# Performance work log

Hardware: AMD Instinct MI355X
Metric: run time of the kernel (lower is better)

## Reference

```python
import jax, jax.numpy as jnp
import numpy as np

R = 512  # rnn_size == att_hid_size == input_encoding_size


def _forward(seq, att_feats, embed_w, W_word, b_word, W_h, b_h, W_img, b_img,
             W_ae, b_ae, W_c2a, b_c2a, W_sl, b_sl, W_se, b_se,
             W_hl, b_hl, W_he, b_he, W_al, b_al, W_a2h, b_a2h, W_log, b_log):
    B, T = seq.shape
    # att_embed: Linear(2048->512) + ReLU  (dropout = identity in eval)
    af = jax.nn.relu(att_feats @ W_ae + b_ae)            # [B,196,R]
    p_att = af @ W_c2a + b_c2a                            # [B,196,R] precomputed attention keys
    img_gate = af.mean(axis=1) @ W_img + b_img            # [B,6R] image contribution to gates (constant over t)
    x_emb = jax.nn.relu(embed_w[seq[:, :T - 1]])          # [B,T-1,R] word embeddings
    wg_t = jnp.swapaxes(x_emb @ W_word + b_word, 0, 1)    # [T-1,B,6R]

    def step(carry, wg):
        hx, cx = carry
        gates = wg + hx @ W_h + b_h + img_gate            # [B,6R]
        sig = jax.nn.sigmoid(gates[:, :4 * R])
        i_g = sig[:, :R]
        f_g = sig[:, R:2 * R]
        o_g = sig[:, 2 * R:3 * R]
        s_g = sig[:, 3 * R:4 * R]
        cell = jnp.maximum(gates[:, 4 * R:5 * R], gates[:, 5 * R:6 * R])
        cy = jnp.tanh(f_g * cx + i_g * cell)
        sent = s_g * cy                                   # visual sentinel
        hy = o_g * cy
        # AdaAttention
        sent_lin = jax.nn.relu(sent @ W_sl + b_sl)        # [B,R]
        sent_emb = sent_lin @ W_se + b_se
        h_lin = jnp.tanh(hy @ W_hl + b_hl)
        h_emb = h_lin @ W_he + b_he
        img_all = jnp.concatenate([sent_lin[:, None, :], af], axis=1)        # [B,197,R]
        img_all_emb = jnp.concatenate([sent_emb[:, None, :], p_att], axis=1)  # [B,197,R]
        hA = jnp.tanh(img_all_emb + h_emb[:, None, :])
        alpha = jax.nn.softmax((hA @ W_al + b_al)[..., 0], axis=-1)           # [B,197]
        cHat = jnp.einsum('ba,bad->bd', alpha, img_all)
        out = jnp.tanh((cHat + h_lin) @ W_a2h + b_a2h)    # [B,R]
        logp = jax.nn.log_softmax(out @ W_log + b_log, axis=-1)  # [B,V]
        return (hy, cy), logp

    h0 = jnp.zeros((B, R), att_feats.dtype)
    _, logps = jax.lax.scan(step, (h0, h0), wg_t)
    return jnp.swapaxes(logps, 0, 1)                      # [B,T-1,V]


def setup_inputs() -> dict:
    B, T, A, FEAT, V = 64, 21, 196, 2048, 7800
    cnt = [0]
    def nk():
        cnt[0] += 1
        return jax.random.fold_in(jax.random.key(0), cnt[0])
    def p(*shape):
        return jax.random.normal(nk(), shape, jnp.float32) * 0.02
    return dict(
        seq=jax.random.randint(nk(), (B, T), 0, V),
        att_feats=jax.random.normal(nk(), (B, A, FEAT), jnp.float32),
        embed_w=p(V, R),
        W_word=p(R, 6 * R), b_word=p(6 * R),
        W_h=p(R, 6 * R), b_h=p(6 * R),
        W_img=p(R, 6 * R), b_img=p(6 * R),
        W_ae=p(FEAT, R), b_ae=p(R),
        W_c2a=p(R, R), b_c2a=p(R),
        W_sl=p(R, R), b_sl=p(R),
        W_se=p(R, R), b_se=p(R),
        W_hl=p(R, R), b_hl=p(R),
        W_he=p(R, R), b_he=p(R),
        W_al=p(R, 1), b_al=p(1),
        W_a2h=p(R, R), b_a2h=p(R),
        W_log=p(R, V), b_log=p(V),
    )


def reference(seq, att_feats, embed_w, W_word, b_word, W_h, b_h, W_img, b_img,
              W_ae, b_ae, W_c2a, b_c2a, W_sl, b_sl, W_se, b_se,
              W_hl, b_hl, W_he, b_he, W_al, b_al, W_a2h, b_a2h, W_log, b_log):
    return _forward(seq, att_feats, embed_w, W_word, b_word, W_h, b_h, W_img, b_img,
                    W_ae, b_ae, W_c2a, b_c2a, W_sl, b_sl, W_se, b_se,
                    W_hl, b_hl, W_he, b_he, W_al, b_al, W_a2h, b_a2h, W_log, b_log)
```

## Files before the change

kernel.cpp:

```cpp
#include <hip/hip_runtime.h>

using short8 = __attribute__((ext_vector_type(8))) short;
using f32x4  = __attribute__((ext_vector_type(4))) float;
typedef unsigned short u16;
typedef unsigned int u32;

__device__ __forceinline__ float b2f(u16 u){
    return __uint_as_float(((u32)u) << 16);
}
__device__ __forceinline__ u16 f2b(float f){
    u32 x = __float_as_uint(f);
    u32 r = (x + 0x7FFFu + ((x >> 16) & 1u)) >> 16;
    return (u16)r;
}
__device__ __forceinline__ float ldx(const void* p, size_t i, bool f32){
    return f32 ? ((const float*)p)[i] : b2f(((const u16*)p)[i]);
}
__device__ __forceinline__ float sigf(float x){
    return __builtin_amdgcn_rcpf(1.0f + __expf(-x));
}
__device__ __forceinline__ float tanhf_(float x){
    float e = __expf(2.0f*x);
    return 1.0f - 2.0f*__builtin_amdgcn_rcpf(e + 1.0f);
}

#define GLDS(g, l) __builtin_amdgcn_global_load_lds((const __attribute__((address_space(1))) void*)(g), \
                        (__attribute__((address_space(3))) void*)(l), 16, 0, 0)

__global__ void probe_dtype(const void* w, int* flag){
    const u16* up = (const u16*)w;
    int lane = threadIdx.x & 63;
    int cnt = 0;
    for (int i = lane; i < 256; i += 64){
        u16 u = up[2*i];
        int e = (u >> 7) & 0xFF;
        if (e >= 100 && e <= 126) cnt++;
    }
    #pragma unroll
    for (int off = 32; off; off >>= 1) cnt += __shfl_xor(cnt, off);
    if (lane == 0) *flag = (cnt >= 192) ? 0 : 1;
}

__global__ __launch_bounds__(256) void convert_att(const void* __restrict__ in, u16* __restrict__ out,
                                                   const int* __restrict__ dflag, int total8){
    bool f32 = (*dflag != 0);
    int i = blockIdx.x*256 + threadIdx.x;
    if (i >= total8) return;
    size_t e = (size_t)i*8;
    if (f32){
        const float4* p = (const float4*)((const float*)in + e);
        float4 v0 = p[0], v1 = p[1];
        u16 o[8] = { f2b(v0.x),f2b(v0.y),f2b(v0.z),f2b(v0.w),
                     f2b(v1.x),f2b(v1.y),f2b(v1.z),f2b(v1.w) };
        *(uint4*)(out + e) = *(const uint4*)o;
    } else {
        *(uint4*)(out + e) = *(const uint4*)((const u16*)in + e);
    }
}

struct TP { const void* src[8]; u16* dst[8]; };
__global__ __launch_bounds__(256) void transpose_multi(TP tp, int K, int N, int Npad,
                                                       const int* __restrict__ dflag){
    __shared__ u16 tile[32][33];
    bool f32 = (*dflag != 0);
    const void* in = tp.src[blockIdx.z];
    u16* out = tp.dst[blockIdx.z];
    int bx = blockIdx.x, by = blockIdx.y;
    int tx = threadIdx.x, ty = threadIdx.y;
    int n = bx*32 + tx;
    #pragma unroll
    for (int i = 0; i < 32; i += 8){
        int k = by*32 + ty + i;
        u16 v = 0;
        if (n < N && k < K)
            v = f32 ? f2b(((const float*)in)[(size_t)k*N + n]) : ((const u16*)in)[(size_t)k*N + n];
        tile[ty+i][tx] = v;
    }
    __syncthreads();
    int k2 = by*32 + tx;
    #pragma unroll
    for (int i = 0; i < 32; i += 8){
        int n2 = bx*32 + ty + i;
        if (n2 < Npad && k2 < K) out[(size_t)n2*K + k2] = tile[tx][ty+i];
    }
}

__global__ __launch_bounds__(256) void gather_emb(const int* __restrict__ seq, const void* __restrict__ embed,
                                                  u16* __restrict__ x_emb, const int* __restrict__ dflag){
    bool f32 = (*dflag != 0);
    int idx = blockIdx.x*256 + threadIdx.x;
    if (idx >= 1280*512) return;
    int row = idx >> 9, r = idx & 511;
    int b = row / 20, t = row % 20;
    int w = seq[b*21 + t];
    float v = ldx(embed, (size_t)w*512 + r, f32);
    x_emb[idx] = f2b(fmaxf(v, 0.f));
}

__global__ __launch_bounds__(256) void mean_af_kernel(const u16* __restrict__ af, u16* __restrict__ mean_af){
    int b = blockIdx.x, tid = threadIdx.x;
    for (int r = tid; r < 512; r += 256){
        float s = 0.f;
        for (int a = 0; a < 196; ++a) s += b2f(af[((size_t)(b*196+a))*512 + r]);
        mean_af[b*512+r] = f2b(s * (1.0f/196.0f));
    }
}

template<int TM>
__global__ __launch_bounds__(256) void gemm_tn(const u16* __restrict__ A, const u16* __restrict__ BT,
                                               int N, int K,
                                               const void* __restrict__ bias1, const void* __restrict__ bias2,
                                               const float* __restrict__ rowAdd, int rowDiv,
                                               float* __restrict__ Cf, u16* __restrict__ Cb,
                                               int act, int Nvalid, int Mvalid,
                                               const int* __restrict__ dflag, int perm){
    constexpr int MW = TM/64;
    __shared__ u16 As[TM*64];
    __shared__ u16 Bs[64*64];
    bool f32 = (*dflag != 0);
    int tid = threadIdx.x, lane = tid & 63, w = tid >> 6;
    int lr = lane & 15, kq = lane >> 4;

    int gN = gridDim.x;
    int nwg = gN * gridDim.y;
    int flat = blockIdx.y*gN + blockIdx.x;
    int q = nwg >> 3, r = nwg & 7;
    int xcd = flat & 7, pos = flat >> 3;
    int wgid = (xcd < r ? xcd*(q+1) : r*(q+1) + (xcd-r)*q) + pos;
    int bm = wgid / gN, bn = wgid % gN;
    int row0 = bm*TM, col0 = bn*64;

    f32x4 acc[MW][4];
    #pragma unroll
    for (int m=0;m<MW;++m)
        #pragma unroll
        for (int n=0;n<4;++n) acc[m][n] = (f32x4){0.f,0.f,0.f,0.f};

    for (int k0 = 0; k0 < K; k0 += 64){
        #pragma unroll
        for (int i=0;i<TM/32;++i){
            int c = i*256 + tid;
            int row = c>>3, slot = (c&7) ^ (row&7);
            GLDS((const char*)A + ((size_t)(row0+row)*K + k0)*2 + slot*16,
                 As + (size_t)(i*256 + w*64)*8);
        }
        #pragma unroll
        for (int i=0;i<2;++i){
            int c = i*256 + tid;
            int row = c>>3, slot = (c&7) ^ (row&7);
            GLDS((const char*)BT + ((size_t)(col0+row)*K + k0)*2 + slot*16,
                 Bs + (size_t)(i*256 + w*64)*8);
        }
        __syncthreads();
        short8 av[MW][2], bv[4][2];
        #pragma unroll
        for (int ks=0;ks<2;++ks){
            #pragma unroll
            for (int m=0;m<MW;++m){
                int rrow = w*(TM/4) + m*16 + lr;
                int sl = (ks*4+kq) ^ (rrow&7);
                av[m][ks] = *(const short8*)(As + rrow*64 + sl*8);
            }
            #pragma unroll
            for (int n=0;n<4;++n){
                int rrow = n*16 + lr;
                int sl = (ks*4+kq) ^ (rrow&7);
                bv[n][ks] = *(const short8*)(Bs + rrow*64 + sl*8);
            }
        }
        #pragma unroll
        for (int ks=0;ks<2;++ks)
            #pragma unroll
            for (int m=0;m<MW;++m)
                #pragma unroll
                for (int n=0;n<4;++n)
                    acc[m][n] = __builtin_amdgcn_mfma_f32_16x16x32_bf16(av[m][ks], bv[n][ks], acc[m][n], 0,0,0);
        __syncthreads();
    }

    #pragma unroll
    for (int n=0;n<4;++n){
        int col = col0 + n*16 + lr;
        float bvv = 0.f;
        if (col < Nvalid){
            if (bias1) bvv += ldx(bias1, col, f32);
            if (bias2) bvv += ldx(bias2, col, f32);
        }
        #pragma unroll
        for (int m=0;m<MW;++m){
            #pragma unroll
            for (int rr=0;rr<4;++rr){
                int row = row0 + w*(TM/4) + m*16 + kq*4 + rr;
                if (row < Mvalid && col < Nvalid){
                    float v = acc[m][n][rr] + bvv;
                    if (rowAdd) v += rowAdd[(size_t)(row/rowDiv)*N + col];
                    if (act == 1) v = fmaxf(v, 0.f);
                    else if (act == 2) v = tanhf_(v);
                    size_t o;
                    if (perm){
                        int orow = (row % 20)*64 + row/20;
                        int ocol = (col & 511)*6 + (col >> 9);
                        o = (size_t)orow*N + ocol;
                    } else {
                        o = (size_t)row*N + col;
                    }
                    if (Cf) Cf[o] = v;
                    if (Cb) Cb[o] = f2b(v);
                }
            }
        }
    }
}

struct GP { const u16* A; const u16* BT; const void* b1; float* Cf; u16* Cb; int act; };
struct GP2 { GP g[2]; };
__global__ __launch_bounds__(256) void gemm_tn2(GP2 ps, int N, int K, int Nvalid, int Mvalid,
                                                const int* __restrict__ dflag){
    __shared__ u16 As[64*64];
    __shared__ u16 Bs[64*64];
    bool f32 = (*dflag != 0);
    GP gp = ps.g[blockIdx.z];
    int tid = threadIdx.x, lane = tid & 63, w = tid >> 6;
    int lr = lane & 15, kq = lane >> 4;

    int gN = gridDim.x;
    int nwg = gN * gridDim.y;
    int flat = blockIdx.y*gN + blockIdx.x;
    int q = nwg >> 3, r = nwg & 7;
    int xcd = flat & 7, pos = flat >> 3;
    int wgid = (xcd < r ? xcd*(q+1) : r*(q+1) + (xcd-r)*q) + pos;
    int bm = wgid / gN, bn = wgid % gN;
    int row0 = bm*64, col0 = bn*64;

    f32x4 acc[4];
    #pragma unroll
    for (int n=0;n<4;++n) acc[n] = (f32x4){0.f,0.f,0.f,0.f};

    for (int k0 = 0; k0 < K; k0 += 64){
        {
            int c = tid;
            int row = c>>3, slot = (c&7) ^ (row&7);
            GLDS((const char*)gp.A + ((size_t)(row0+row)*K + k0)*2 + slot*16,
                 As + (size_t)(w*64)*8);
            c = 256 + tid;
            row = c>>3; slot = (c&7) ^ (row&7);
            GLDS((const char*)gp.A + ((size_t)(row0+row)*K + k0)*2 + slot*16,
                 As + (size_t)(256 + w*64)*8);
            c = tid;
            row = c>>3; slot = (c&7) ^ (row&7);
            GLDS((const char*)gp.BT + ((size_t)(col0+row)*K + k0)*2 + slot*16,
                 Bs + (size_t)(w*64)*8);
            c = 256 + tid;
            row = c>>3; slot = (c&7) ^ (row&7);
            GLDS((const char*)gp.BT + ((size_t)(col0+row)*K + k0)*2 + slot*16,
                 Bs + (size_t)(256 + w*64)*8);
        }
        __syncthreads();
        short8 av[2], bv[4][2];
        #pragma unroll
        for (int ks=0;ks<2;++ks){
            int rrow = w*16 + lr;
            int sl = (ks*4+kq) ^ (rrow&7);
            av[ks] = *(const short8*)(As + rrow*64 + sl*8);
            #pragma unroll
            for (int n=0;n<4;++n){
                int rr2 = n*16 + lr;
                int sl2 = (ks*4+kq) ^ (rr2&7);
                bv[n][ks] = *(const short8*)(Bs + rr2*64 + sl2*8);
            }
        }
        #pragma unroll
        for (int ks=0;ks<2;++ks)
            #pragma unroll
            for (int n=0;n<4;++n)
                acc[n] = __builtin_amdgcn_mfma_f32_16x16x32_bf16(av[ks], bv[n][ks], acc[n], 0,0,0);
        __syncthreads();
    }

    #pragma unroll
    for (int n=0;n<4;++n){
        int col = col0 + n*16 + lr;
        float bvv = (col < Nvalid && gp.b1) ? ldx(gp.b1, col, f32) : 0.f;
        #pragma unroll
        for (int rr=0;rr<4;++rr){
            int row = row0 + w*16 + kq*4 + rr;
            if (row < Mvalid && col < Nvalid){
                float v = acc[n][rr] + bvv;
                if (gp.act == 1) v = fmaxf(v, 0.f);
                else if (gp.act == 2) v = tanhf_(v);
                size_t o = (size_t)row*N + col;
                if (gp.Cf) gp.Cf[o] = v;
                if (gp.Cb) gp.Cb[o] = f2b(v);
            }
        }
    }
}

#define GP3 52
__global__ __launch_bounds__(192) void lstm_step(const u16* __restrict__ h_in, const u16* __restrict__ WT_h,
                                                 const float* __restrict__ wgb, float* __restrict__ cstate,
                                                 u16* __restrict__ h_out, u16* __restrict__ sent_all,
                                                 u16* __restrict__ hy_all, int t){
    __shared__ float gates[16*GP3];
    int tid = threadIdx.x, lane = tid & 63, w = tid >> 6;
    int mg = blockIdx.x >> 6, rg = blockIdx.x & 63;
    int b0 = mg*16, r0 = rg*8;
    int lr = lane & 15, kq = lane >> 4, kg = kq*8;
    int c = w*16 + lr;
    int gate = c >> 3, rcol = r0 + (c & 7);
    const u16* Ap = h_in + (size_t)(b0 + lr)*512 + kg;
    const u16* Bp = WT_h + ((size_t)gate*512 + rcol)*512 + kg;
    f32x4 acc = (f32x4){0.f,0.f,0.f,0.f};
    #pragma unroll
    for (int k0 = 0; k0 < 512; k0 += 32){
        short8 a  = *(const short8*)(Ap + k0);
        short8 bf = *(const short8*)(Bp + k0);
        acc = __builtin_amdgcn_mfma_f32_16x16x32_bf16(a, bf, acc, 0,0,0);
    }
    #pragma unroll
    for (int rr = 0; rr < 4; ++rr)
        gates[(kq*4+rr)*GP3 + c] = acc[rr];
    __syncthreads();
    if (tid < 128){
        int ri = tid >> 3, rr = tid & 7;
        int b = b0 + ri, r = r0 + rr;
        const float* wp = wgb + (((size_t)t*64 + b)*512 + r)*6;
        float2 w01 = *(const float2*)(wp);
        float2 w23 = *(const float2*)(wp + 2);
        float2 w45 = *(const float2*)(wp + 4);
        float g0 = gates[ri*GP3 +      rr] + w01.x;
        float g1 = gates[ri*GP3 +  8 + rr] + w01.y;
        float g2 = gates[ri*GP3 + 16 + rr] + w23.x;
        float g3 = gates[ri*GP3 + 24 + rr] + w23.y;
        float g4 = gates[ri*GP3 + 32 + rr] + w45.x;
        float g5 = gates[ri*GP3 + 40 + rr] + w45.y;
        float ig = sigf(g0), fg = sigf(g1), og = sigf(g2), sg = sigf(g3);
        float cell = fmaxf(g4, g5);
        float co = cstate[b*512 + r];
        float cy = tanhf_(fg*co + ig*cell);
        cstate[b*512 + r] = cy;
        float sent = sg*cy, hy = og*cy;
        h_out[(size_t)b*512 + r] = f2b(hy);
        size_t rgl = (size_t)b*20 + t;
        sent_all[rgl*512 + r] = f2b(sent);
        hy_all[rgl*512 + r]   = f2b(hy);
    }
}

__global__ __launch_bounds__(256) void attn_kernel(const u16* __restrict__ sembb, const float* __restrict__ h_emb,
                                                   const float* __restrict__ sent_lin_f, const float* __restrict__ h_lin_f,
                                                   const u16* __restrict__ p_att, const u16* __restrict__ af,
                                                   const void* __restrict__ W_al, const void* __restrict__ b_al,
                                                   u16* __restrict__ ctx_in, const int* __restrict__ dflag){
    __shared__ float he_s[512];
    __shared__ float wal_s[512];
    __shared__ float se_s[512];
    __shared__ float ev[208];
    __shared__ float red2[2];
    bool f32 = (*dflag != 0);
    int flat = blockIdx.x;
    int row = (flat & 7)*160 + (flat >> 3);
    int b = row / 20;
    int tid = threadIdx.x, lane = tid & 63, w = tid >> 6;
    for (int d = tid; d < 512; d += 256){
        int ad = ((d & 7) >> 1)*128 + (d >> 3)*2 + (d & 1);
        he_s[ad]  = h_emb[(size_t)row*512 + d];
        wal_s[ad] = ldx(W_al, d, f32);
        se_s[ad]  = b2f(sembb[(size_t)row*512 + d]);
    }
    __syncthreads();
    float bal = ldx(b_al, 0, f32);

    if (w == 0){
        float p0 = 0.f;
        #pragma unroll
        for (int jp = 0; jp < 4; ++jp){
            float2 he2 = *(const float2*)&he_s[jp*128 + lane*2];
            float2 wa2 = *(const float2*)&wal_s[jp*128 + lane*2];
            float2 se2 = *(const float2*)&se_s[jp*128 + lane*2];
            p0 += tanhf_(se2.x + he2.x) * wa2.x;
            p0 += tanhf_(se2.y + he2.y) * wa2.y;
        }
        #pragma unroll
        for (int off = 32; off; off >>= 1) p0 += __shfl_xor(p0, off);
        if (lane == 0) ev[0] = p0 + bal;
    }

    const u16* pb = p_att + (size_t)b*196*512 + lane*8;
    for (int a = 1 + w; a < 197; a += 8){
        bool has2 = (a + 4 < 197);
        const u16* r0 = pb + (size_t)(a-1)*512;
        short8 v0 = *(const short8*)r0;
        short8 v1 = has2 ? *(const short8*)(r0 + (size_t)4*512) : v0;
        const u32* pk0 = (const u32*)&v0;
        const u32* pk1 = (const u32*)&v1;
        float p0 = 0.f, p1 = 0.f;
        #pragma unroll
        for (int jp = 0; jp < 4; ++jp){
            float2 he2 = *(const float2*)&he_s[jp*128 + lane*2];
            float2 wa2 = *(const float2*)&wal_s[jp*128 + lane*2];
            u32 u0 = pk0[jp], u1 = pk1[jp];
            float x00 = __uint_as_float(u0 << 16)          + he2.x;
            float x01 = __uint_as_float(u0 & 0xFFFF0000u)  + he2.y;
            float x10 = __uint_as_float(u1 << 16)          + he2.x;
            float x11 = __uint_as_float(u1 & 0xFFFF0000u)  + he2.y;
            p0 += tanhf_(x00)*wa2.x;
            p0 += tanhf_(x01)*wa2.y;
            p1 += tanhf_(x10)*wa2.x;
            p1 += tanhf_(x11)*wa2.y;
        }
        #pragma unroll
        for (int off = 32; off; off >>= 1){
            p0 += __shfl_xor(p0, off);
            p1 += __shfl_xor(p1, off);
        }
        if (lane == 0){
            ev[a] = p0 + bal;
            if (has2) ev[a+4] = p1 + bal;
        }
    }
    __syncthreads();

    if (w == 0){
        float m = -1e30f;
        for (int a = lane; a < 197; a += 64) m = fmaxf(m, ev[a]);
        #pragma unroll
        for (int off = 32; off; off >>= 1) m = fmaxf(m, __shfl_xor(m, off));
        float s = 0.f;
        for (int a = lane; a < 197; a += 64) s += __expf(ev[a] - m);
        #pragma unroll
        for (int off = 32; off; off >>= 1) s += __shfl_xor(s, off);
        if (lane == 0){ red2[0] = m; red2[1] = __builtin_amdgcn_rcpf(s); }
    }
    __syncthreads();
    float m = red2[0], inv = red2[1];
    for (int a = tid; a < 197; a += 256) ev[a] = __expf(ev[a] - m) * inv;
    __syncthreads();

    int d = tid*2;
    const u16* afb = af + (size_t)b*196*512 + d;
    float s0 = 0.f, s1 = 0.f, t0 = 0.f, t1 = 0.f;
    for (int a = 0; a < 196; a += 2){
        float e0 = ev[a+1], e1 = ev[a+2];
        u32 u0 = *(const u32*)(afb + (size_t)a*512);
        u32 u1 = *(const u32*)(afb + (size_t)(a+1)*512);
        s0 += e0 * __uint_as_float(u0 << 16);
        s1 += e0 * __uint_as_float(u0 & 0xFFFF0000u);
        t0 += e1 * __uint_as_float(u1 << 16);
        t1 += e1 * __uint_as_float(u1 & 0xFFFF0000u);
    }
    float e00 = ev[0];
    float a0 = e00*sent_lin_f[(size_t)row*512 + d]     + s0 + t0 + h_lin_f[(size_t)row*512 + d];
    float a1 = e00*sent_lin_f[(size_t)row*512 + d + 1] + s1 + t1 + h_lin_f[(size_t)row*512 + d + 1];
    ctx_in[(size_t)row*512 + d]     = f2b(a0);
    ctx_in[(size_t)row*512 + d + 1] = f2b(a1);
}

__global__ __launch_bounds__(256) void logsoftmax_kernel(const u16* __restrict__ logits, void* __restrict__ out,
                                                         const int* __restrict__ dflag){
    __shared__ float red[256];
    bool f32 = (*dflag != 0);
    int row = blockIdx.x, tid = threadIdx.x;
    const u16* lp = logits + (size_t)row*7808;
    float m = -1e30f;
    for (int v = tid; v < 7800; v += 256) m = fmaxf(m, b2f(lp[v]));
    red[tid] = m; __syncthreads();
    for (int s = 128; s; s >>= 1){ if (tid < s) red[tid] = fmaxf(red[tid], red[tid+s]); __syncthreads(); }
    m = red[0]; __syncthreads();
    float s = 0.f;
    for (int v = tid; v < 7800; v += 256) s += __expf(b2f(lp[v]) - m);
    red[tid] = s; __syncthreads();
    for (int st = 128; st; st >>= 1){ if (tid < st) red[tid] += red[tid+st]; __syncthreads(); }
    float lse = m + __logf(red[0]);
    if (f32){
        float* op = (float*)out + (size_t)row*7800;
        for (int v = tid; v < 7800; v += 256) op[v] = b2f(lp[v]) - lse;
    } else {
        u16* op = (u16*)out + (size_t)row*7800;
        for (int v = tid; v < 7800; v += 256) op[v] = f2b(b2f(lp[v]) - lse);
    }
}

extern "C" void kernel_launch(void* const* d_in, const int* in_sizes, int n_in,
                              void* d_out, int out_size, void* d_ws, size_t ws_size,
                              hipStream_t stream){
    (void)in_sizes; (void)n_in; (void)out_size; (void)ws_size;
    const int* seq    = (const int*)d_in[0];
    const void* att   = d_in[1];
    const void* embed = d_in[2];
    const void* W_word= d_in[3];  const void* b_word = d_in[4];
    const void* W_h   = d_in[5];  const void* b_h    = d_in[6];
    const void* W_img = d_in[7];  const void* b_img  = d_in[8];
    const void* W_ae  = d_in[9];  const void* b_ae   = d_in[10];
    const void* W_c2a = d_in[11]; const void* b_c2a  = d_in[12];
    const void* W_sl  = d_in[13]; const void* b_sl   = d_in[14];
    const void* W_se  = d_in[15]; const void* b_se   = d_in[16];
    const void* W_hl  = d_in[17]; const void* b_hl   = d_in[18];
    const void* W_he  = d_in[19]; const void* b_he   = d_in[20];
    const void* W_al  = d_in[21]; const void* b_al   = d_in[22];
    const void* W_a2h = d_in[23]; const void* b_a2h  = d_in[24];
    const void* W_log = d_in[25]; const void* b_log  = d_in[26];

    char* p = (char*)d_ws;
    auto alloc = [&](size_t bytes)->char*{ char* r = p; p += (bytes + 255) & ~(size_t)255; return r; };

    int* dflag   = (int*)alloc(256);
    u16* WT_ae   = (u16*)alloc((size_t)512*2048*2);
    u16* WT_word = (u16*)alloc((size_t)3072*512*2);
    u16* WT_h    = (u16*)alloc((size_t)3072*512*2);
    u16* WT_img  = (u16*)alloc((size_t)3072*512*2);
    u16* WT_c2a  = (u16*)alloc((size_t)512*512*2);
    u16* WT_sl   = (u16*)alloc((size_t)512*512*2);
    u16* WT_se   = (u16*)alloc((size_t)512*512*2);
    u16* WT_hl   = (u16*)alloc((size_t)512*512*2);
    u16* WT_he   = (u16*)alloc((size_t)512*512*2);
    u16* WT_a2h  = (u16*)alloc((size_t)512*512*2);
    u16* WT_log  = (u16*)alloc((size_t)7808*512*2);
    u16* af      = (u16*)alloc((size_t)12544*512*2);
    u16* p_att   = (u16*)alloc((size_t)12544*512*2);
    u16* meanb   = (u16*)alloc((size_t)64*512*2);
    float* imgg  = (float*)alloc((size_t)64*3072*4);
    u16* xemb    = (u16*)alloc((size_t)1280*512*2);
    float* wgb   = (float*)alloc((size_t)1280*3072*4);
    u16* hb0     = (u16*)alloc((size_t)64*512*2);
    u16* hb1     = (u16*)alloc((size_t)64*512*2);
    float* cst   = (float*)alloc((size_t)64*512*4);
    u16* sent_all= (u16*)alloc((size_t)1280*512*2);
    u16* hy_all  = (u16*)alloc((size_t)1280*512*2);
    float* slf   = (float*)alloc((size_t)1280*512*4);
    u16* slb     = (u16*)alloc((size_t)1280*512*2);
    float* hlf   = (float*)alloc((size_t)1280*512*4);
    u16* hlb     = (u16*)alloc((size_t)1280*512*2);
    u16* sembb   = (u16*)alloc((size_t)1280*512*2);
    float* hemb  = (float*)alloc((size_t)1280*512*4);
    u16* ctx     = (u16*)alloc((size_t)1280*512*2);
    u16* a2hb    = (u16*)alloc((size_t)1280*512*2);
    u16* logits  = (u16*)alloc((size_t)1280*7808*2);

    u16* attb = (u16*)wgb;

    probe_dtype<<<1, 64, 0, stream>>>(W_ae, dflag);

    dim3 tb(32,8);
    {
        TP t6{};
        t6.src[0]=W_c2a; t6.dst[0]=WT_c2a;
        t6.src[1]=W_sl;  t6.dst[1]=WT_sl;
        t6.src[2]=W_se;  t6.dst[2]=WT_se;
        t6.src[3]=W_hl;  t6.dst[3]=WT_hl;
        t6.src[4]=W_he;  t6.dst[4]=WT_he;
        t6.src[5]=W_a2h; t6.dst[5]=WT_a2h;
        transpose_multi<<<dim3(16,16,6), tb, 0, stream>>>(t6, 512, 512, 512, dflag);
        TP t3{};
        t3.src[0]=W_word; t3.dst[0]=WT_word;
        t3.src[1]=W_h;    t3.dst[1]=WT_h;
        t3.src[2]=W_img;  t3.dst[2]=WT_img;
        transpose_multi<<<dim3(96,16,3), tb, 0, stream>>>(t3, 512, 3072, 3072, dflag);
        TP ta{}; ta.src[0]=W_ae; ta.dst[0]=WT_ae;
        transpose_multi<<<dim3(16,64,1), tb, 0, stream>>>(ta, 2048, 512, 512, dflag);
        TP tl{}; tl.src[0]=W_log; tl.dst[0]=WT_log;
        transpose_multi<<<dim3(244,16,1), tb, 0, stream>>>(tl, 512, 7800, 7808, dflag);
    }

    convert_att<<<12544, 256, 0, stream>>>(att, attb, dflag, 12544*2048/8);

    gemm_tn<128><<<dim3(8,98), 256, 0, stream>>>(attb, WT_ae, 512, 2048,
                                                 b_ae, nullptr, nullptr, 1, nullptr, af, 1, 512, 12544, dflag, 0);
    gemm_tn<128><<<dim3(8,98), 256, 0, stream>>>(af, WT_c2a, 512, 512,
                                                 b_c2a, nullptr, nullptr, 1, nullptr, p_att, 0, 512, 12544, dflag, 0);
    mean_af_kernel<<<64, 256, 0, stream>>>(af, meanb);
    gemm_tn<64><<<dim3(48,1), 256, 0, stream>>>(meanb, WT_img, 3072, 512,
                                                b_img, nullptr, nullptr, 1, imgg, nullptr, 0, 3072, 64, dflag, 0);
    gather_emb<<<2560, 256, 0, stream>>>(seq, embed, xemb, dflag);
    gemm_tn<64><<<dim3(48,20), 256, 0, stream>>>(xemb, WT_word, 3072, 512,
                                                 b_word, b_h, imgg, 20, wgb, nullptr, 0, 3072, 1280, dflag, 1);

    hipMemsetAsync(hb0, 0, (size_t)64*512*2, stream);
    hipMemsetAsync(cst, 0, (size_t)64*512*4, stream);

    for (int t = 0; t < 20; ++t){
        const u16* hin = (t & 1) ? hb1 : hb0;
        u16* hout      = (t & 1) ? hb0 : hb1;
        lstm_step<<<256, 192, 0, stream>>>(hin, WT_h, wgb, cst, hout, sent_all, hy_all, t);
    }

    GP2 pa{};
    pa.g[0] = { sent_all, WT_sl, b_sl, slf, slb, 1 };
    pa.g[1] = { hy_all,   WT_hl, b_hl, hlf, hlb, 2 };
    gemm_tn2<<<dim3(8,20,2), 256, 0, stream>>>(pa, 512, 512, 512, 1280, dflag);
    GP2 pb{};
    pb.g[0] = { slb, WT_se, b_se, nullptr, sembb, 0 };
    pb.g[1] = { hlb, WT_he, b_he, hemb, nullptr, 0 };
    gemm_tn2<<<dim3(8,20,2), 256, 0, stream>>>(pb, 512, 512, 512, 1280, dflag);

    attn_kernel<<<1280, 256, 0, stream>>>(sembb, hemb, slf, hlf, p_att, af, W_al, b_al, ctx, dflag);
    gemm_tn<64><<<dim3(8,20), 256, 0, stream>>>(ctx, WT_a2h, 512, 512,
                                                b_a2h, nullptr, nullptr, 1, nullptr, a2hb, 2, 512, 1280, dflag, 0);
    gemm_tn<128><<<dim3(122,10), 256, 0, stream>>>(a2hb, WT_log, 7808, 512,
                                                   b_log, nullptr, nullptr, 1, nullptr, logits, 0, 7800, 1280, dflag, 0);
    logsoftmax_kernel<<<1280, 256, 0, stream>>>(logits, d_out, dflag);
}
```

Before: 423.3 us.

## Fuse fp32-to-bf16 conversion into att_embed GEMM, tabulate tanh, cache logits

Removes the separate convert_att pass. A new gemm_af kernel loads fp32 att_feats straight into LDS and packs them to bf16 in registers before the MFMA, which saves a full write and reread of the large converted buffer. The attention kernel replaces its exp-based tanh with a 512-entry LDS lookup table and linear interpolation. The log-softmax kernel keeps each row's logits in registers so the row is read once instead of three times. The table-based tanh is an approximation that loses some accuracy, and the new GEMM uses 64-row tiles without software pipelining, which may cost GEMM efficiency.

```diff
diff --git a/kernel.cpp b/kernel.cpp
--- a/kernel.cpp
+++ b/kernel.cpp
@@ -22,6 +22,11 @@
 __device__ __forceinline__ float tanhf_(float x){
     float e = __expf(2.0f*x);
     return 1.0f - 2.0f*__builtin_amdgcn_rcpf(e + 1.0f);
+}
+__device__ __forceinline__ u32 cvtpk(float lo, float hi){
+    u32 r;
+    asm("v_cvt_pk_bf16_f32 %0, %1, %2" : "=v"(r) : "v"(lo), "v"(hi));
+    return r;
 }
 
 #define GLDS(g, l) __builtin_amdgcn_global_load_lds((const __attribute__((address_space(1))) void*)(g), \
@@ -39,23 +44,6 @@
     #pragma unroll
     for (int off = 32; off; off >>= 1) cnt += __shfl_xor(cnt, off);
     if (lane == 0) *flag = (cnt >= 192) ? 0 : 1;
-}
-
-__global__ __launch_bounds__(256) void convert_att(const void* __restrict__ in, u16* __restrict__ out,
-                                                   const int* __restrict__ dflag, int total8){
-    bool f32 = (*dflag != 0);
-    int i = blockIdx.x*256 + threadIdx.x;
-    if (i >= total8) return;
-    size_t e = (size_t)i*8;
-    if (f32){
-        const float4* p = (const float4*)((const float*)in + e);
-        float4 v0 = p[0], v1 = p[1];
-        u16 o[8] = { f2b(v0.x),f2b(v0.y),f2b(v0.z),f2b(v0.w),
-                     f2b(v1.x),f2b(v1.y),f2b(v1.z),f2b(v1.w) };
-        *(uint4*)(out + e) = *(const uint4*)o;
-    } else {
-        *(uint4*)(out + e) = *(const uint4*)((const u16*)in + e);
-    }
 }
 
 struct TP { const void* src[8]; u16* dst[8]; };
@@ -103,6 +91,112 @@
         float s = 0.f;
         for (int a = 0; a < 196; ++a) s += b2f(af[((size_t)(b*196+a))*512 + r]);
         mean_af[b*512+r] = f2b(s * (1.0f/196.0f));
+    }
+}
+
+__global__ __launch_bounds__(256) void gemm_af(const void* __restrict__ A, const u16* __restrict__ BT,
+                                               int N, int K, const void* __restrict__ bias1,
+                                               u16* __restrict__ Cb, int Nvalid, int Mvalid,
+                                               const int* __restrict__ dflag){
+    __shared__ char AsRaw[64*64*4];
+    __shared__ u16 Bs[64*64];
+    bool f32 = (*dflag != 0);
+    float* Asf = (float*)AsRaw;
+    u16* As16 = (u16*)AsRaw;
+    int tid = threadIdx.x, lane = tid & 63, w = tid >> 6;
+    int lr = lane & 15, kq = lane >> 4;
+
+    int gN = gridDim.x;
+    int nwg = gN * gridDim.y;
+    int flat = blockIdx.y*gN + blockIdx.x;
+    int q = nwg >> 3, r = nwg & 7;
+    int xcd = flat & 7, pos = flat >> 3;
+    int wgid = (xcd < r ? xcd*(q+1) : r*(q+1) + (xcd-r)*q) + pos;
+    int bm = wgid / gN, bn = wgid % gN;
+    int row0 = bm*64, col0 = bn*64;
+
+    f32x4 acc[4];
+    #pragma unroll
+    for (int n=0;n<4;++n) acc[n] = (f32x4){0.f,0.f,0.f,0.f};
+
+    for (int k0 = 0; k0 < K; k0 += 64){
+        if (f32){
+            const float* Af = (const float*)A;
+            #pragma unroll
+            for (int i=0;i<4;++i){
+                int c = i*256 + tid;
+                int row = c >> 4, sslot = c & 15;
+                int srcslot = sslot ^ ((row & 7) << 1);
+                GLDS((const char*)(Af + (size_t)(row0+row)*K + k0) + srcslot*16,
+                     Asf + (size_t)(i*256 + w*64)*4);
+            }
+        } else {
+            const u16* Ab = (const u16*)A;
+            #pragma unroll
+            for (int i=0;i<2;++i){
+                int c = i*256 + tid;
+                int row = c>>3, slot = (c&7) ^ (row&7);
+                GLDS((const char*)(Ab + (size_t)(row0+row)*K + k0) + slot*16,
+                     As16 + (size_t)(i*256 + w*64)*8);
+            }
+        }
+        #pragma unroll
+        for (int i=0;i<2;++i){
+            int c = i*256 + tid;
+            int row = c>>3, slot = (c&7) ^ (row&7);
+            GLDS((const char*)BT + ((size_t)(col0+row)*K + k0)*2 + slot*16,
+                 Bs + (size_t)(i*256 + w*64)*8);
+        }
+        __syncthreads();
+        short8 av[2], bv[4][2];
+        int rrow = w*16 + lr;
+        if (f32){
+            int m8 = (rrow & 7) << 1;
+            #pragma unroll
+            for (int ks=0;ks<2;++ks){
+                int j = ks*4 + kq;
+                float4 lo = *(const float4*)&Asf[rrow*64 + ((2*j)^m8)*4];
+                float4 hi = *(const float4*)&Asf[rrow*64 + ((2*j+1)^m8)*4];
+                u32 pk[4] = { cvtpk(lo.x,lo.y), cvtpk(lo.z,lo.w),
+                              cvtpk(hi.x,hi.y), cvtpk(hi.z,hi.w) };
+                av[ks] = *(const short8*)pk;
+            }
+        } else {
+            #pragma unroll
+            for (int ks=0;ks<2;++ks){
+                int sl = (ks*4+kq) ^ (rrow&7);
+                av[ks] = *(const short8*)(As16 + rrow*64 + sl*8);
+            }
+        }
+        #pragma unroll
+        for (int ks=0;ks<2;++ks){
+            #pragma unroll
+            for (int n=0;n<4;++n){
+                int rr2 = n*16 + lr;
+                int sl2 = (ks*4+kq) ^ (rr2&7);
+                bv[n][ks] = *(const short8*)(Bs + rr2*64 + sl2*8);
+            }
+        }
+        #pragma unroll
+        for (int ks=0;ks<2;++ks)
+            #pragma unroll
+            for (int n=0;n<4;++n)
+                acc[n] = __builtin_amdgcn_mfma_f32_16x16x32_bf16(av[ks], bv[n][ks], acc[n], 0,0,0);
+        __syncthreads();
+    }
+
+    #pragma unroll
+    for (int n=0;n<4;++n){
+        int col = col0 + n*16 + lr;
+        float bvv = (col < Nvalid && bias1) ? ldx(bias1, col, f32) : 0.f;
+        #pragma unroll
+        for (int rr=0;rr<4;++rr){
+            int row = row0 + w*16 + kq*4 + rr;
+            if (row < Mvalid && col < Nvalid){
+                float v = fmaxf(acc[n][rr] + bvv, 0.f);
+                Cb[(size_t)row*N + col] = f2b(v);
+            }
+        }
     }
 }
 
@@ -352,6 +446,7 @@
                                                    const u16* __restrict__ p_att, const u16* __restrict__ af,
                                                    const void* __restrict__ W_al, const void* __restrict__ b_al,
                                                    u16* __restrict__ ctx_in, const int* __restrict__ dflag){
+    __shared__ float tab[512];
     __shared__ float he_s[512];
     __shared__ float wal_s[512];
     __shared__ float se_s[512];
@@ -362,6 +457,8 @@
     int row = (flat & 7)*160 + (flat >> 3);
     int b = row / 20;
     int tid = threadIdx.x, lane = tid & 63, w = tid >> 6;
+    #pragma unroll
+    for (int i = tid; i < 512; i += 256) tab[i] = tanhf((i - 256) * 0.03125f);
     for (int d = tid; d < 512; d += 256){
         int ad = ((d & 7) >> 1)*128 + (d >> 3)*2 + (d & 1);
         he_s[ad]  = h_emb[(size_t)row*512 + d];
@@ -371,6 +468,15 @@
     __syncthreads();
     float bal = ldx(b_al, 0, f32);
 
+    auto tanh_t = [&](float x)->float{
+        float xc = fminf(fmaxf(x, -7.9f), 7.9f);
+        float fi = __fmaf_rn(xc, 32.0f, 256.0f);
+        int ii = (int)fi;
+        float fr = fi - (float)ii;
+        float t0 = tab[ii], t1 = tab[ii+1];
+        return __fmaf_rn(fr, t1 - t0, t0);
+    };
+
     if (w == 0){
         float p0 = 0.f;
         #pragma unroll
@@ -378,8 +484,8 @@
             float2 he2 = *(const float2*)&he_s[jp*128 + lane*2];
             float2 wa2 = *(const float2*)&wal_s[jp*128 + lane*2];
             float2 se2 = *(const float2*)&se_s[jp*128 + lane*2];
-            p0 += tanhf_(se2.x + he2.x) * wa2.x;
-            p0 += tanhf_(se2.y + he2.y) * wa2.y;
+            p0 += tanh_t(se2.x + he2.x) * wa2.x;
+            p0 += tanh_t(se2.y + he2.y) * wa2.y;
         }
         #pragma unroll
         for (int off = 32; off; off >>= 1) p0 += __shfl_xor(p0, off);
@@ -404,10 +510,10 @@
             float x01 = __uint_as_float(u0 & 0xFFFF0000u)  + he2.y;
             float x10 = __uint_as_float(u1 << 16)          + he2.x;
             float x11 = __uint_as_float(u1 & 0xFFFF0000u)  + he2.y;
-            p0 += tanhf_(x00)*wa2.x;
-            p0 += tanhf_(x01)*wa2.y;
-            p1 += tanhf_(x10)*wa2.x;
-            p1 += tanhf_(x11)*wa2.y;
+            p0 += tanh_t(x00)*wa2.x;
+            p0 += tanh_t(x01)*wa2.y;
+            p1 += tanh_t(x10)*wa2.x;
+            p1 += tanh_t(x11)*wa2.y;
         }
         #pragma unroll
         for (int off = 32; off; off >>= 1){
@@ -462,22 +568,37 @@
     bool f32 = (*dflag != 0);
     int row = blockIdx.x, tid = threadIdx.x;
     const u16* lp = logits + (size_t)row*7808;
+    float xs[31];
     float m = -1e30f;
-    for (int v = tid; v < 7800; v += 256) m = fmaxf(m, b2f(lp[v]));
+    #pragma unroll
+    for (int k = 0; k < 31; ++k){
+        int v = k*256 + tid;
+        xs[k] = (v < 7800) ? b2f(lp[v]) : -1e30f;
+        m = fmaxf(m, xs[k]);
+    }
     red[tid] = m; __syncthreads();
     for (int s = 128; s; s >>= 1){ if (tid < s) red[tid] = fmaxf(red[tid], red[tid+s]); __syncthreads(); }
     m = red[0]; __syncthreads();
     float s = 0.f;
-    for (int v = tid; v < 7800; v += 256) s += __expf(b2f(lp[v]) - m);
+    #pragma unroll
+    for (int k = 0; k < 31; ++k) s += __expf(xs[k] - m);
     red[tid] = s; __syncthreads();
     for (int st = 128; st; st >>= 1){ if (tid < st) red[tid] += red[tid+st]; __syncthreads(); }
     float lse = m + __logf(red[0]);
     if (f32){
         float* op = (float*)out + (size_t)row*7800;
-        for (int v = tid; v < 7800; v += 256) op[v] = b2f(lp[v]) - lse;
+        #pragma unroll
+        for (int k = 0; k < 31; ++k){
+            int v = k*256 + tid;
+            if (v < 7800) op[v] = xs[k] - lse;
+        }
     } else {
         u16* op = (u16*)out + (size_t)row*7800;
-        for (int v = tid; v < 7800; v += 256) op[v] = f2b(b2f(lp[v]) - lse);
+        #pragma unroll
+        for (int k = 0; k < 31; ++k){
+            int v = k*256 + tid;
+            if (v < 7800) op[v] = f2b(xs[k] - lse);
+        }
     }
 }
 
@@ -537,8 +658,6 @@
     u16* a2hb    = (u16*)alloc((size_t)1280*512*2);
     u16* logits  = (u16*)alloc((size_t)1280*7808*2);
 
-    u16* attb = (u16*)wgb;
-
     probe_dtype<<<1, 64, 0, stream>>>(W_ae, dflag);
 
     dim3 tb(32,8);
@@ -562,10 +681,7 @@
         transpose_multi<<<dim3(244,16,1), tb, 0, stream>>>(tl, 512, 7800, 7808, dflag);
     }
 
-    convert_att<<<12544, 256, 0, stream>>>(att, attb, dflag, 12544*2048/8);
-
-    gemm_tn<128><<<dim3(8,98), 256, 0, stream>>>(attb, WT_ae, 512, 2048,
-                                                 b_ae, nullptr, nullptr, 1, nullptr, af, 1, 512, 12544, dflag, 0);
+    gemm_af<<<dim3(8,196), 256, 0, stream>>>(att, WT_ae, 512, 2048, b_ae, af, 512, 12544, dflag);
     gemm_tn<128><<<dim3(8,98), 256, 0, stream>>>(af, WT_c2a, 512, 512,
                                                  b_c2a, nullptr, nullptr, 1, nullptr, p_att, 0, 512, 12544, dflag, 0);
     mean_af_kernel<<<64, 256, 0, stream>>>(af, meanb);
```

Measured after the change: 428.0 us. Within noise of the previous version (+1.1%).
